# Performance work log

Measured on AMD Instinct MI355X. Metric: run time of the kernel, lower is better.

## Reference

```python
import jax, jax.numpy as jnp
import numpy as np

B, J, C, K, TOK, CH = 4096, 17, 512, 3, 256, 2048
EPS = 1e-5


def layernorm(x, g, b):
    m = jnp.mean(x, axis=-1, keepdims=True)
    v = jnp.mean(jnp.square(x - m), axis=-1, keepdims=True)
    return (x - m) / jnp.sqrt(v + EPS) * g + b


def gcn(x_bcj, W, b, adj):
    # 1x1 conv to K*C channels: (b,c,v) x (k,o,c) -> (b,k,o,v), then adjacency mix over v
    y = jnp.einsum('bcv,koc->bkov', x_bcj, W) + b[None, :, :, None]
    return jnp.einsum('bkov,kvw->bow', y, adj)  # (b, C, J)


def mlp(x, W1, b1, W2, b2):
    # torch Linear: y = x @ W.T + b ; GELU is exact (erf) in torch default
    h = jax.nn.gelu(x @ W1.T + b1, approximate=False)
    return h @ W2.T + b2


def setup_inputs() -> dict:
    key = jax.random.key(0)
    ks = jax.random.split(key, 8)
    s = lambda fan: 1.0 / np.sqrt(fan)
    return {
        'x': jax.random.normal(ks[0], (B, J, C), jnp.float32),
        'adj': jax.random.uniform(ks[1], (K, J, J), jnp.float32),
        'g1': jnp.ones((J,), jnp.float32), 'be1': jnp.zeros((J,), jnp.float32),
        'g2': jnp.ones((C,), jnp.float32), 'be2': jnp.zeros((C,), jnp.float32),
        'Wg1': jax.random.normal(ks[2], (K, C, C), jnp.float32) * s(C),
        'bg1': jnp.zeros((K, C), jnp.float32),
        'Wg2': jax.random.normal(ks[3], (K, C, C), jnp.float32) * s(C),
        'bg2': jnp.zeros((K, C), jnp.float32),
        'W11': jax.random.normal(ks[4], (TOK, J), jnp.float32) * s(J),
        'b11': jnp.zeros((TOK,), jnp.float32),
        'W12': jax.random.normal(ks[5], (J, TOK), jnp.float32) * s(TOK),
        'b12': jnp.zeros((J,), jnp.float32),
        'W21': jax.random.normal(ks[6], (CH, C), jnp.float32) * s(C),
        'b21': jnp.zeros((CH,), jnp.float32),
        'W22': jax.random.normal(ks[7], (C, CH), jnp.float32) * s(CH),
        'b22': jnp.zeros((C,), jnp.float32),
    }


def reference(x, adj, g1, be1, g2, be2, Wg1, bg1, Wg2, bg2,
              W11, b11, W12, b12, W21, b21, W22, b22):
    # model_type == 'graph_mlp'
    xt = jnp.transpose(x, (0, 2, 1))          # (B, C, J)
    res = xt
    xn = layernorm(xt, g1, be1)               # LN over J (length)
    g1_out = gcn(xn, Wg1, bg1, adj)           # (B, C, J)
    xt = res + mlp(xn, W11, b11, W12, b12) + g1_out
    x2 = jnp.transpose(xt, (0, 2, 1))         # (B, J, C)
    res = x2
    xn = layernorm(x2, g2, be2)               # LN over C (dim)
    g2_out = gcn(jnp.transpose(xn, (0, 2, 1)), Wg2, bg2, adj)  # (B, C, J)
    out = res + mlp(xn, W21, b21, W22, b22) + jnp.transpose(g2_out, (0, 2, 1))
    return out
```

## Files before the change

### kernel.cpp

```cpp
#include <hip/hip_runtime.h>
#include <hip/hip_bf16.h>

#define Bn   4096
#define Jn   17
#define Cn   512
#define Kn   3
#define TOKn 256
#define CHn  2048
#define EPSf 1e-5f
#define Mrows (Bn * Jn)
#define KCAT (CHn + Kn * Cn)

typedef unsigned short u16;
typedef short bf8_t __attribute__((ext_vector_type(8)));
typedef float f32x4 __attribute__((ext_vector_type(4)));

__device__ __forceinline__ float gelu_fast(float x) {
    float x2 = x * x;
    float z = x * __builtin_fmaf(0.1029474f, x2, 2.3022652f);
    float e = __builtin_amdgcn_exp2f(z);
    float r = __builtin_amdgcn_rcpf(e + 1.0f);
    return x * (1.0f - r);
}
__device__ __forceinline__ float bf2f(u16 u) {
    union { float f; unsigned int i; } w; w.i = ((unsigned int)u) << 16; return w.f;
}
__device__ __forceinline__ u16 f2bf(float f) {
    __hip_bfloat16 h = __float2bfloat16(f);
    union { __hip_bfloat16 h1; u16 u; } cv; cv.h1 = h; return cv.u;
}
__device__ __forceinline__ unsigned pk2(float a, float b) {
    float2 t; t.x = a; t.y = b;
    __hip_bfloat162 h = __float22bfloat162_rn(t);
    union { __hip_bfloat162 h2; unsigned u; } cv; cv.h2 = h; return cv.u;
}
__device__ __forceinline__ void unpack2(unsigned u, float& a, float& b) {
    union { float f; unsigned int i; } t;
    t.i = u << 16;          a = t.f;
    t.i = u & 0xffff0000u;  b = t.f;
}
__device__ __forceinline__ void gload_lds16(const void* g, void* l) {
    __builtin_amdgcn_global_load_lds(
        (const __attribute__((address_space(1))) void*)g,
        (__attribute__((address_space(3))) void*)l, 16, 0, 0);
}

__global__ __launch_bounds__(256) void prep_kernel(
    const float* __restrict__ W21, const float* __restrict__ W22,
    const float* __restrict__ Wg1, const float* __restrict__ Wg2,
    const float* __restrict__ bg1, const float* __restrict__ bg2,
    const float* __restrict__ adj,
    const float* __restrict__ W11, const float* __restrict__ W12,
    const float* __restrict__ b22,
    u16* __restrict__ W21b, u16* __restrict__ W22b,
    u16* __restrict__ Wg1t, u16* __restrict__ Wg2t,
    float* __restrict__ bias2a, float* __restrict__ bias2b, float* __restrict__ bias2bc,
    u16* __restrict__ W11p, u16* __restrict__ W12p,
    u16* __restrict__ Wcomb)
{
    int bid = blockIdx.x, tid = threadIdx.x;
    if (bid < 1024) {
        const float* src = (bid < 512) ? W21 : W22;
        u16* dst = (bid < 512) ? W21b : W22b;
        size_t base = (size_t)(bid & 511) * 2048 + (size_t)tid * 8;
        float4 v0 = *(const float4*)(src + base);
        float4 v1 = *(const float4*)(src + base + 4);
        uint4 o;
        o.x = pk2(v0.x, v0.y); o.y = pk2(v0.z, v0.w);
        o.z = pk2(v1.x, v1.y); o.w = pk2(v1.z, v1.w);
        *(uint4*)(dst + base) = o;
    } else if (bid < 2048) {
        const float* src = (bid < 1536) ? Wg1 : Wg2;
        u16* dst = (bid < 1536) ? Wg1t : Wg2t;
        int rbase = ((bid - 1024) & 511) * 3;
        int c = tid * 2;
        for (int rr = 0; rr < 3; ++rr) {
            int ro = rbase + rr;
            int k = ro >> 9, o = ro & 511;
            const float* sp = src + ((size_t)k * Cn + o) * Cn + c;
            float2 v = *(const float2*)sp;
            *(unsigned*)(dst + (size_t)o * (Kn * Cn) + k * Cn + c) = pk2(v.x, v.y);
        }
    } else if (bid == 2048) {
        __shared__ float adjcs[Kn][Jn];
        for (int i = tid; i < Kn * Jn; i += 256) {
            int k = i / Jn, w = i - k * Jn;
            float s = 0.f;
            for (int v = 0; v < Jn; ++v) s += adj[k * (Jn * Jn) + v * Jn + w];
            adjcs[k][w] = s;
        }
        __syncthreads();
        for (int i = tid; i < Jn * Cn; i += 256) {
            int w = i >> 9, o = i & 511;
            float sa = 0.f, sb = 0.f;
            #pragma unroll
            for (int k = 0; k < Kn; ++k) {
                sa += bg1[k * Cn + o] * adjcs[k][w];
                sb += bg2[k * Cn + o] * adjcs[k][w];
            }
            bias2a[i] = sa; bias2b[i] = sb; bias2bc[i] = sb + b22[o];
        }
    } else if (bid == 2049) {
        for (int i = tid; i < 4 * TOKn * 8; i += 256) {
            int ck = i >> 11, t = (i >> 3) & 255, e = i & 7;
            int k = ck * 8 + e;
            W11p[i] = (k < Jn) ? f2bf(W11[t * Jn + k]) : (u16)0;
        }
        for (int idx = tid; idx < 32 * TOKn; idx += 256) {
            int j = idx >> 8, t = idx & 255;
            W12p[idx] = (j < Jn) ? f2bf(W12[j * TOKn + t]) : (u16)0;
        }
    } else {
        int o = bid - 2050;
        for (int idx = tid; idx < KCAT; idx += 256) {
            float v;
            if (idx < CHn) v = W22[(size_t)o * CHn + idx];
            else {
                int rem = idx - CHn;
                int k = rem >> 9, c = rem & 511;
                v = Wg2[((size_t)k * Cn + o) * Cn + c];
            }
            Wcomb[(size_t)o * KCAT + idx] = f2bf(v);
        }
    }
}

template<int STAGE>
__global__ __launch_bounds__(256) void premix_kernel(
    const float* __restrict__ x,
    const u16* __restrict__ xn2,
    const float* __restrict__ adj,
    const float* __restrict__ g1, const float* __restrict__ be1,
    float* __restrict__ mean1, float* __restrict__ rstd1,
    u16* __restrict__ xmix, int oStride, int oColOff)
{
    __shared__ float xsh[Jn][Cn];
    __shared__ float coef[Kn][Jn][Jn];
    __shared__ float s0sh[Kn][Jn];
    __shared__ float s1sh[Kn][Jn];
    __shared__ float msh[Cn], rsh[Cn];
    int b = blockIdx.x, tid = threadIdx.x;

    for (int i = tid; i < Kn * Jn * Jn; i += 256) {
        int k = i / (Jn * Jn); int rem = i - k * (Jn * Jn);
        int v = rem / Jn; int w = rem - v * Jn;
        float av = adj[i];
        coef[k][w][v] = (STAGE == 1) ? av * g1[v] : av;
    }
    if (STAGE == 1) {
        const float* xp = x + (size_t)b * (Jn * Cn);
        for (int i = tid; i < (Jn * Cn) / 4; i += 256)
            ((float4*)&xsh[0][0])[i] = ((const float4*)xp)[i];
    } else {
        const u16* xp = xn2 + (size_t)b * (Jn * Cn);
        for (int i = tid; i < (Jn * Cn) / 8; i += 256) {
            uint4 u = ((const uint4*)xp)[i];
            float* d = &(&xsh[0][0])[i * 8];
            unpack2(u.x, d[0], d[1]); unpack2(u.y, d[2], d[3]);
            unpack2(u.z, d[4], d[5]); unpack2(u.w, d[6], d[7]);
        }
    }
    __syncthreads();
    if (STAGE == 1) {
        for (int c = tid; c < Cn; c += 256) {
            float s = 0.f, q = 0.f;
            #pragma unroll
            for (int v = 0; v < Jn; ++v) { float t = xsh[v][c]; s += t; q += t * t; }
            float m = s * (1.0f / Jn);
            float var = fmaxf(q * (1.0f / Jn) - m * m, 0.f);
            float r = rsqrtf(var + EPSf);
            msh[c] = m; rsh[c] = r;
            mean1[(size_t)b * Cn + c] = m;
            rstd1[(size_t)b * Cn + c] = r;
        }
    }
    if (tid < Kn * Jn) {
        int k = tid / Jn, w = tid - k * Jn;
        float s0 = 0.f, s1 = 0.f;
        #pragma unroll
        for (int v = 0; v < Jn; ++v) {
            if (STAGE == 1) s0 += adj[k * (Jn * Jn) + v * Jn + w] * be1[v];
            s1 += coef[k][w][v];
        }
        s0sh[k][w] = s0; s1sh[k][w] = s1;
    }
    __syncthreads();
    u16* orow = xmix + (size_t)b * Jn * oStride + oColOff;
    int c = tid * 2;
    float m0v = 0.f, m1v = 0.f, r0v = 1.f, r1v = 1.f;
    if (STAGE == 1) { m0v = msh[c]; m1v = msh[c + 1]; r0v = rsh[c]; r1v = rsh[c + 1]; }
    for (int k = 0; k < Kn; ++k)
        for (int w = 0; w < Jn; ++w) {
            float cf[Jn];
            #pragma unroll
            for (int v = 0; v < Jn; ++v) cf[v] = coef[k][w][v];
            float d0 = 0.f, d1 = 0.f;
            #pragma unroll
            for (int v = 0; v < Jn; ++v) { d0 += cf[v] * xsh[v][c]; d1 += cf[v] * xsh[v][c + 1]; }
            float v0, v1;
            if (STAGE == 1) {
                float ss1 = s1sh[k][w], ss0 = s0sh[k][w];
                v0 = r0v * (d0 - m0v * ss1) + ss0;
                v1 = r1v * (d1 - m1v * ss1) + ss0;
            } else { v0 = d0; v1 = d1; }
            *(unsigned*)(orow + (size_t)w * oStride + k * Cn + c) = pk2(v0, v1);
        }
}

__global__ __launch_bounds__(512) void mlp1_mfma(
    const float* __restrict__ x,
    const float* __restrict__ mean1, const float* __restrict__ rstd1,
    const float* __restrict__ g1, const float* __restrict__ be1,
    const u16* __restrict__ W11p,
    const float* __restrict__ b11,
    const u16* __restrict__ W12p,
    const float* __restrict__ b12,
    float* __restrict__ out)
{
    __shared__ __align__(16) u16 As[128 * 40];
    __shared__ __align__(16) u16 Hs[128 * 128];
    __shared__ __align__(16) u16 W11s[4 * TOKn * 8];
    __shared__ __align__(16) u16 W12s[32 * TOKn];
    __shared__ __align__(16) float b11s[TOKn];
    __shared__ __align__(16) float msrs[256];
    __shared__ float g1s[32], be1s[32];

    int tid = threadIdx.x;
    int lane = tid & 63, wave = tid >> 6;
    int li = lane & 15, q = lane >> 4;
    int b = blockIdx.y, c0 = blockIdx.x * 128;
    const float* xb = x + (size_t)b * (Jn * Cn);

    #pragma unroll
    for (int t = 0; t < 2; ++t) {
        int idx = t * 512 + tid;
        gload_lds16(W11p + idx * 8, (char*)W11s + idx * 16);
    }
    #pragma unroll
    for (int t = 0; t < 2; ++t) {
        int idx = t * 512 + tid;
        int j = idx >> 5, s = idx & 31;
        gload_lds16(W12p + j * TOKn + ((s ^ (j & 7)) << 3), (char*)W12s + idx * 16);
    }
    if (wave == 0) gload_lds16(b11 + lane * 4, (char*)b11s + lane * 16);
    if (wave == 1) {
        const float* src = (lane < 32) ? (mean1 + (size_t)b * Cn + c0 + lane * 4)
                                       : (rstd1 + (size_t)b * Cn + c0 + (lane - 32) * 4);
        gload_lds16(src, (char*)msrs + lane * 16);
    }
    if (tid < Jn) { g1s[tid] = g1[tid]; be1s[tid] = be1[tid]; }
    asm volatile("s_waitcnt vmcnt(0)" ::: "memory");
    __syncthreads();

    const float* ms = msrs;
    const float* rs = msrs + 128;
    #pragma unroll
    for (int it = 0; it < 4; ++it) {
        int idx = it * 512 + tid;
        int r = idx & 127, k = (idx >> 7) << 1;
        float mr = ms[r], rr = rs[r];
        float v0 = 0.f, v1 = 0.f;
        if (k < Jn)     v0 = (xb[(size_t)k * Cn + c0 + r] - mr) * rr * g1s[k] + be1s[k];
        if (k + 1 < Jn) v1 = (xb[(size_t)(k + 1) * Cn + c0 + r] - mr) * rr * g1s[k + 1] + be1s[k + 1];
        int ck = (k >> 3) ^ ((r >> 3) & 3);
        *(unsigned*)((char*)As + r * 80 + (ck << 4) + ((k & 7) << 1)) = pk2(v0, v1);
    }
    __syncthreads();

    int wbase = wave * 16;
    f32x4 acc2[2];
    acc2[0] = (f32x4)0.f; acc2[1] = (f32x4)0.f;

    bf8_t bfc;
    {
        int c = wbase + li;
        int ck = q ^ ((c >> 3) & 3);
        bfc = *(const bf8_t*)((const char*)As + c * 80 + (ck << 4));
    }

    #pragma unroll
    for (int ch = 0; ch < 2; ++ch) {
        f32x4 acc1[8];
        #pragma unroll
        for (int tf = 0; tf < 8; ++tf) acc1[tf] = (f32x4)0.f;
        #pragma unroll
        for (int tf = 0; tf < 8; ++tf) {
            int t = ch * 128 + tf * 16 + li;
            bf8_t aw = *(const bf8_t*)((const char*)W11s + (q << 12) + t * 16);
            acc1[tf] = __builtin_amdgcn_mfma_f32_16x16x32_bf16(aw, bfc, acc1[tf], 0, 0, 0);
        }
        #pragma unroll
        for (int tf = 0; tf < 8; ++tf) {
            int t0 = tf * 16 + (q << 2);
            float bq0 = b11s[ch * 128 + t0 + 0];
            float bq1 = b11s[ch * 128 + t0 + 1];
            float bq2 = b11s[ch * 128 + t0 + 2];
            float bq3 = b11s[ch * 128 + t0 + 3];
            int c = wbase + li;
            float h0 = gelu_fast(acc1[tf][0] + bq0);
            float h1 = gelu_fast(acc1[tf][1] + bq1);
            float h2 = gelu_fast(acc1[tf][2] + bq2);
            float h3 = gelu_fast(acc1[tf][3] + bq3);
            uint2 w; w.x = pk2(h0, h1); w.y = pk2(h2, h3);
            *(uint2*)((char*)Hs + c * 256 + ((((t0 >> 3) ^ (c & 7))) << 4) + ((t0 & 7) << 1)) = w;
        }
        #pragma unroll
        for (int kt = 0; kt < 4; ++kt) {
            int c = wbase + li;
            int tc = kt * 4 + q;
            bf8_t bh = *(const bf8_t*)((const char*)Hs + c * 256 + ((tc ^ (c & 7)) << 4));
            #pragma unroll
            for (int jf = 0; jf < 2; ++jf) {
                int j = jf * 16 + li;
                int tcg = ch * 16 + kt * 4 + q;
                bf8_t aw = *(const bf8_t*)((const char*)W12s + j * 512 + ((tcg ^ (j & 7)) << 4));
                acc2[jf] = __builtin_amdgcn_mfma_f32_16x16x32_bf16(aw, bh, acc2[jf], 0, 0, 0);
            }
        }
    }

    #pragma unroll
    for (int jf = 0; jf < 2; ++jf) {
        int c = c0 + wbase + li;
        #pragma unroll
        for (int i = 0; i < 4; ++i) {
            int j = jf * 16 + (q << 2) + i;
            if (j < Jn) {
                size_t off = (size_t)b * (Jn * Cn) + (size_t)j * Cn + c;
                out[off] = x[off] + acc2[jf][i] + b12[j];
            }
        }
    }
}

__global__ __launch_bounds__(256) void ln2_kernel(const float* __restrict__ X2,
        const float* __restrict__ g2, const float* __restrict__ be2,
        u16* __restrict__ xn2)
{
    int row = blockIdx.x * 4 + (threadIdx.x >> 6);
    int lane = threadIdx.x & 63;
    const float* p = X2 + (size_t)row * Cn;
    float4 v0 = ((const float4*)p)[lane];
    float4 v1 = ((const float4*)p)[lane + 64];
    float s = v0.x + v0.y + v0.z + v0.w + v1.x + v1.y + v1.z + v1.w;
    float q = v0.x*v0.x + v0.y*v0.y + v0.z*v0.z + v0.w*v0.w
            + v1.x*v1.x + v1.y*v1.y + v1.z*v1.z + v1.w*v1.w;
    #pragma unroll
    for (int off = 32; off > 0; off >>= 1) { s += __shfl_xor(s, off); q += __shfl_xor(q, off); }
    float mean = s * (1.0f / Cn);
    float var = fmaxf(q * (1.0f / Cn) - mean * mean, 0.f);
    float rs = rsqrtf(var + EPSf);
    float4 ga = ((const float4*)g2)[lane],      ba = ((const float4*)be2)[lane];
    float4 gb = ((const float4*)g2)[lane + 64], bb = ((const float4*)be2)[lane + 64];
    uint2 w0, w1;
    w0.x = pk2((v0.x-mean)*rs*ga.x + ba.x, (v0.y-mean)*rs*ga.y + ba.y);
    w0.y = pk2((v0.z-mean)*rs*ga.z + ba.z, (v0.w-mean)*rs*ga.w + ba.w);
    w1.x = pk2((v1.x-mean)*rs*gb.x + bb.x, (v1.y-mean)*rs*gb.y + bb.y);
    w1.y = pk2((v1.z-mean)*rs*gb.z + bb.z, (v1.w-mean)*rs*gb.w + bb.w);
    ((uint2*)(xn2 + (size_t)row * Cn))[lane] = w0;
    ((uint2*)(xn2 + (size_t)row * Cn))[lane + 64] = w1;
}

template<int EPI>
__global__ __launch_bounds__(256, 4) void gemm_bt(
    const u16* __restrict__ A, int ldA,
    const u16* __restrict__ Bt, int ldB,
    int K, int ldOut,
    const float* __restrict__ bias,
    float* __restrict__ outF, u16* __restrict__ outH)
{
    __shared__ __align__(16) u16 As[2][128 * 32];
    __shared__ __align__(16) u16 Bs[2][128 * 32];
    int tid = threadIdx.x;
    int gx = gridDim.x;
    int total = gx * gridDim.y;
    int lid = blockIdx.y * gx + blockIdx.x;
    int cpx = total >> 3;
    int wg = (lid & 7) * cpx + (lid >> 3);
    int n0 = (wg % gx) << 7;
    int m0 = (wg / gx) << 7;

    int wave = tid >> 6, lane = tid & 63;
    int wr = wave >> 1, wc = wave & 1;

    const u16* aSrc[2]; const u16* bSrc[2];
    #pragma unroll
    for (int t = 0; t < 2; ++t) {
        int idx = t * 256 + tid;
        int r = idx >> 2;
        int cs = (idx & 3) ^ ((r >> 1) & 3);
        aSrc[t] = A  + (size_t)(m0 + r) * ldA + cs * 8;
        bSrc[t] = Bt + (size_t)(n0 + r) * ldB + cs * 8;
    }
    int aOff[4], bOff[4];
    #pragma unroll
    for (int i = 0; i < 4; ++i) {
        int ra = wr * 64 + i * 16 + (lane & 15);
        aOff[i] = ra * 64 + ((((lane >> 4)) ^ ((ra >> 1) & 3)) << 4);
        int rb = wc * 64 + i * 16 + (lane & 15);
        bOff[i] = rb * 64 + ((((lane >> 4)) ^ ((rb >> 1) & 3)) << 4);
    }

    f32x4 acc[4][4];
    #pragma unroll
    for (int i = 0; i < 4; ++i)
        #pragma unroll
        for (int j = 0; j < 4; ++j) acc[i][j] = (f32x4)0.f;

    int KT = K >> 5;
    #pragma unroll
    for (int t = 0; t < 2; ++t) {
        int idx = t * 256 + tid;
        gload_lds16(aSrc[t], (char*)&As[0][0] + idx * 16);
        gload_lds16(bSrc[t], (char*)&Bs[0][0] + idx * 16);
    }
    int cur = 0;
    for (int kt = 0; kt < KT; ++kt) {
        asm volatile("s_waitcnt vmcnt(0)" ::: "memory");
        __syncthreads();
        if (kt + 1 < KT) {
            int k0 = (kt + 1) << 5;
            #pragma unroll
            for (int t = 0; t < 2; ++t) {
                int idx = t * 256 + tid;
                gload_lds16(aSrc[t] + k0, (char*)&As[cur ^ 1][0] + idx * 16);
                gload_lds16(bSrc[t] + k0, (char*)&Bs[cur ^ 1][0] + idx * 16);
            }
        }
        bf8_t af[4], bfr[4];
        #pragma unroll
        for (int i = 0; i < 4; ++i) {
            af[i]  = *(const bf8_t*)((const char*)&As[cur][0] + aOff[i]);
            bfr[i] = *(const bf8_t*)((const char*)&Bs[cur][0] + bOff[i]);
        }
        #pragma unroll
        for (int mi = 0; mi < 4; ++mi)
            #pragma unroll
            for (int ni = 0; ni < 4; ++ni)
                acc[mi][ni] = __builtin_amdgcn_mfma_f32_16x16x32_bf16(af[mi], bfr[ni], acc[mi][ni], 0, 0, 0);
        cur ^= 1;
    }

    #pragma unroll
    for (int mi = 0; mi < 4; ++mi) {
        int rbase = m0 + wr * 64 + mi * 16 + ((lane >> 4) << 2);
        #pragma unroll
        for (int ni = 0; ni < 4; ++ni) {
            int col = n0 + wc * 64 + ni * 16 + (lane & 15);
            if (EPI == 0) {
                float bv = bias[col];
                #pragma unroll
                for (int i = 0; i < 4; ++i) {
                    float v = gelu_fast(acc[mi][ni][i] + bv);
                    outH[(size_t)(rbase + i) * ldOut + col] = f2bf(v);
                }
            } else if (EPI == 1) {
                float bv = bias ? bias[col] : 0.f;
                #pragma unroll
                for (int i = 0; i < 4; ++i) {
                    size_t off = (size_t)(rbase + i) * ldOut + col;
                    outF[off] += acc[mi][ni][i] + bv;
                }
            } else {
                #pragma unroll
                for (int i = 0; i < 4; ++i) {
                    int row = rbase + i;
                    int w = row % Jn;
                    size_t off = (size_t)row * ldOut + col;
                    outF[off] += acc[mi][ni][i] + bias[w * Cn + col];
                }
            }
        }
    }
}

extern "C" void kernel_launch(void* const* d_in, const int* in_sizes, int n_in,
                              void* d_out, int out_size, void* d_ws, size_t ws_size,
                              hipStream_t stream)
{
    (void)in_sizes; (void)n_in; (void)out_size;
    const float* x   = (const float*)d_in[0];
    const float* adj = (const float*)d_in[1];
    const float* g1  = (const float*)d_in[2];
    const float* be1 = (const float*)d_in[3];
    const float* g2  = (const float*)d_in[4];
    const float* be2 = (const float*)d_in[5];
    const float* Wg1 = (const float*)d_in[6];
    const float* bg1 = (const float*)d_in[7];
    const float* Wg2 = (const float*)d_in[8];
    const float* bg2 = (const float*)d_in[9];
    const float* W11 = (const float*)d_in[10];
    const float* b11 = (const float*)d_in[11];
    const float* W12 = (const float*)d_in[12];
    const float* b12 = (const float*)d_in[13];
    const float* W21 = (const float*)d_in[14];
    const float* b21 = (const float*)d_in[15];
    const float* W22 = (const float*)d_in[16];
    const float* b22 = (const float*)d_in[17];
    float* out = (float*)d_out;

    char* p = (char*)d_ws;
    float* mean1  = (float*)p;                 p += (size_t)Bn * Cn * 4;
    float* rstd1  = (float*)p;                 p += (size_t)Bn * Cn * 4;
    u16*   xn2    = (u16*)p;                   p += (size_t)Mrows * Cn * 2;
    u16*   W21b   = (u16*)p;                   p += (size_t)CHn * Cn * 2;
    u16*   W22b   = (u16*)p;                   p += (size_t)CHn * Cn * 2;
    u16*   Wg1t   = (u16*)p;                   p += (size_t)Cn * Kn * Cn * 2;
    u16*   Wg2t   = (u16*)p;                   p += (size_t)Cn * Kn * Cn * 2;
    u16*   Wcomb  = (u16*)p;                   p += (size_t)Cn * KCAT * 2;
    float* bias2a = (float*)p;                 p += (size_t)Jn * Cn * 4;
    float* bias2b = (float*)p;                 p += (size_t)Jn * Cn * 4;
    float* bias2bc= (float*)p;                 p += (size_t)Jn * Cn * 4;
    u16*   W11p   = (u16*)p;                   p += (size_t)4 * TOKn * 8 * 2;
    u16*   W12p   = (u16*)p;                   p += (size_t)32 * TOKn * 2;
    u16*   xmix   = (u16*)p;
    u16*   Hbuf   = xmix;

    size_t fixedBytes = (size_t)((char*)xmix - (char*)d_ws);
    bool combined = ws_size >= fixedBytes + (size_t)Mrows * KCAT * 2;
    bool fullH    = ws_size >= fixedBytes + (size_t)Mrows * CHn * 2;

    prep_kernel<<<2562, 256, 0, stream>>>(W21, W22, Wg1, Wg2, bg1, bg2, adj, W11, W12, b22,
                                          W21b, W22b, Wg1t, Wg2t, bias2a, bias2b, bias2bc,
                                          W11p, W12p, Wcomb);
    premix_kernel<1><<<Bn, 256, 0, stream>>>(x, (const u16*)nullptr, adj, g1, be1, mean1, rstd1,
                                             xmix, Kn * Cn, 0);
    {
        dim3 g(Cn / 128, Bn);
        mlp1_mfma<<<g, 512, 0, stream>>>(x, mean1, rstd1, g1, be1, W11p, b11, W12p, b12, out);
    }
    {
        dim3 g(Cn / 128, Mrows / 128);
        gemm_bt<2><<<g, 256, 0, stream>>>(xmix, Kn * Cn, Wg1t, Kn * Cn, Kn * Cn, Cn, bias2a, out, (u16*)nullptr);
    }
    ln2_kernel<<<Mrows / 4, 256, 0, stream>>>(out, g2, be2, xn2);
    if (combined) {
        u16* HX = xmix;
        {
            dim3 ga(CHn / 128, Mrows / 128);
            gemm_bt<0><<<ga, 256, 0, stream>>>(xn2, Cn, W21b, Cn, Cn, KCAT, b21, (float*)nullptr, HX);
        }
        premix_kernel<2><<<Bn, 256, 0, stream>>>((const float*)nullptr, xn2, adj, (const float*)nullptr,
                                                 (const float*)nullptr, (float*)nullptr, (float*)nullptr,
                                                 HX, KCAT, CHn);
        {
            dim3 g(Cn / 128, Mrows / 128);
            gemm_bt<2><<<g, 256, 0, stream>>>(HX, KCAT, Wcomb, KCAT, KCAT, Cn, bias2bc, out, (u16*)nullptr);
        }
    } else {
        if (fullH) {
            dim3 ga(CHn / 128, Mrows / 128);
            gemm_bt<0><<<ga, 256, 0, stream>>>(xn2, Cn, W21b, Cn, Cn, CHn, b21, (float*)nullptr, Hbuf);
            dim3 gb(Cn / 128, Mrows / 128);
            gemm_bt<1><<<gb, 256, 0, stream>>>(Hbuf, CHn, W22b, CHn, CHn, Cn, b22, out, (u16*)nullptr);
        } else {
            for (int h = 0; h < 2; ++h) {
                int hc = h * 1024;
                dim3 ga(1024 / 128, Mrows / 128);
                gemm_bt<0><<<ga, 256, 0, stream>>>(xn2, Cn, W21b + (size_t)hc * Cn, Cn, Cn, 1024, b21 + hc, (float*)nullptr, Hbuf);
                dim3 gb(Cn / 128, Mrows / 128);
                gemm_bt<1><<<gb, 256, 0, stream>>>(Hbuf, 1024, W22b + hc, CHn, 1024, Cn, (h == 0) ? b22 : (const float*)nullptr, out, (u16*)nullptr);
            }
        }
        premix_kernel<2><<<Bn, 256, 0, stream>>>((const float*)nullptr, xn2, adj, (const float*)nullptr,
                                                 (const float*)nullptr, (float*)nullptr, (float*)nullptr,
                                                 xmix, Kn * Cn, 0);
        {
            dim3 g(Cn / 128, Mrows / 128);
            gemm_bt<2><<<g, 256, 0, stream>>>(xmix, Kn * Cn, Wg2t, Kn * Cn, Kn * Cn, Cn, bias2b, out, (u16*)nullptr);
        }
    }
}
```

Baseline: 1.549 ms.

## Triple-buffer GEMM LDS tiles with partial vmcnt waits for deeper prefetch

```diff
diff --git a/kernel.cpp b/kernel.cpp
--- a/kernel.cpp
+++ b/kernel.cpp
@@ -362,15 +362,15 @@
 }
 
 template<int EPI>
-__global__ __launch_bounds__(256, 4) void gemm_bt(
+__global__ __launch_bounds__(256, 3) void gemm_bt(
     const u16* __restrict__ A, int ldA,
     const u16* __restrict__ Bt, int ldB,
     int K, int ldOut,
     const float* __restrict__ bias,
     float* __restrict__ outF, u16* __restrict__ outH)
 {
-    __shared__ __align__(16) u16 As[2][128 * 32];
-    __shared__ __align__(16) u16 Bs[2][128 * 32];
+    __shared__ __align__(16) u16 As[3 * 128 * 32];
+    __shared__ __align__(16) u16 Bs[3 * 128 * 32];
     int tid = threadIdx.x;
     int gx = gridDim.x;
     int total = gx * gridDim.y;
@@ -384,6 +384,7 @@
     int wr = wave >> 1, wc = wave & 1;
 
     const u16* aSrc[2]; const u16* bSrc[2];
+    int ldsOff[2];
     #pragma unroll
     for (int t = 0; t < 2; ++t) {
         int idx = t * 256 + tid;
@@ -391,6 +392,7 @@
         int cs = (idx & 3) ^ ((r >> 1) & 3);
         aSrc[t] = A  + (size_t)(m0 + r) * ldA + cs * 8;
         bSrc[t] = Bt + (size_t)(n0 + r) * ldB + cs * 8;
+        ldsOff[t] = idx * 16;
     }
     int aOff[4], bOff[4];
     #pragma unroll
@@ -409,36 +411,51 @@
 
     int KT = K >> 5;
     #pragma unroll
-    for (int t = 0; t < 2; ++t) {
-        int idx = t * 256 + tid;
-        gload_lds16(aSrc[t], (char*)&As[0][0] + idx * 16);
-        gload_lds16(bSrc[t], (char*)&Bs[0][0] + idx * 16);
-    }
-    int cur = 0;
-    for (int kt = 0; kt < KT; ++kt) {
-        asm volatile("s_waitcnt vmcnt(0)" ::: "memory");
-        __syncthreads();
-        if (kt + 1 < KT) {
-            int k0 = (kt + 1) << 5;
+    for (int sl = 0; sl < 2; ++sl) {
+        int k0 = sl << 5;
+        #pragma unroll
+        for (int t = 0; t < 2; ++t) {
+            gload_lds16(aSrc[t] + k0, (char*)As + sl * 8192 + ldsOff[t]);
+            gload_lds16(bSrc[t] + k0, (char*)Bs + sl * 8192 + ldsOff[t]);
+        }
+    }
+
+    int slot = 0;
+    int pslot = 2;
+    for (int s = 0; s < KT; ++s) {
+        if (s + 2 < KT) {
+            int k0 = (s + 2) << 5;
             #pragma unroll
             for (int t = 0; t < 2; ++t) {
-                int idx = t * 256 + tid;
-                gload_lds16(aSrc[t] + k0, (char*)&As[cur ^ 1][0] + idx * 16);
-                gload_lds16(bSrc[t] + k0, (char*)&Bs[cur ^ 1][0] + idx * 16);
-            }
-        }
+                gload_lds16(aSrc[t] + k0, (char*)As + pslot * 8192 + ldsOff[t]);
+                gload_lds16(bSrc[t] + k0, (char*)Bs + pslot * 8192 + ldsOff[t]);
+            }
+        }
+        int rem = KT - 1 - s;
+        if (rem >= 2)      asm volatile("s_waitcnt vmcnt(8)" ::: "memory");
+        else if (rem == 1) asm volatile("s_waitcnt vmcnt(4)" ::: "memory");
+        else               asm volatile("s_waitcnt vmcnt(0)" ::: "memory");
+        __builtin_amdgcn_s_barrier();
+
+        const char* aBase = (const char*)As + slot * 8192;
+        const char* bBase = (const char*)Bs + slot * 8192;
         bf8_t af[4], bfr[4];
         #pragma unroll
         for (int i = 0; i < 4; ++i) {
-            af[i]  = *(const bf8_t*)((const char*)&As[cur][0] + aOff[i]);
-            bfr[i] = *(const bf8_t*)((const char*)&Bs[cur][0] + bOff[i]);
+            af[i]  = *(const bf8_t*)(aBase + aOff[i]);
+            bfr[i] = *(const bf8_t*)(bBase + bOff[i]);
         }
         #pragma unroll
         for (int mi = 0; mi < 4; ++mi)
             #pragma unroll
             for (int ni = 0; ni < 4; ++ni)
                 acc[mi][ni] = __builtin_amdgcn_mfma_f32_16x16x32_bf16(af[mi], bfr[ni], acc[mi][ni], 0, 0, 0);
-        cur ^= 1;
+        asm volatile("s_waitcnt lgkmcnt(0)" ::: "memory");
+        __builtin_amdgcn_sched_barrier(0);
+        __builtin_amdgcn_s_barrier();
+
+        slot = (slot == 2) ? 0 : slot + 1;
+        pslot = (pslot == 2) ? 0 : pslot + 1;
     }
 
     #pragma unroll
```

Result: no change. 1.557 ms (+0.5%).
